# Optimization experiments

Measured on AMD Instinct MI355X. Metric: run time of the kernel, lower is better.

Reference implementation:

```python
import jax, jax.numpy as jnp
import numpy as np

DEPTH = 4
N_MOLS = 2000
ATOMS_PER_MOL = 50
N_ATOMS = N_MOLS * ATOMS_PER_MOL + 1   # +1 zero-padding row (chemprop convention)
N_BONDS = 200001                        # +1 zero-padding row
MAX_NB = 6
ATOM_FDIM, BOND_FDIM, HIDDEN = 133, 147, 300


def setup_inputs() -> dict:
    key = jax.random.key(0)
    ks = jax.random.split(key, 12)
    f_atoms = jax.random.uniform(ks[0], (N_ATOMS, ATOM_FDIM), jnp.float32).at[0].set(0.0)
    f_bonds = jax.random.uniform(ks[1], (N_BONDS, BOND_FDIM), jnp.float32).at[0].set(0.0)
    w_atoms = jax.random.uniform(ks[2], (N_ATOMS,), jnp.float32) + 0.5
    w_bonds = (jax.random.uniform(ks[3], (N_BONDS,), jnp.float32) + 0.5).at[0].set(0.0)
    a2b = jax.random.randint(ks[4], (N_ATOMS, MAX_NB), 0, N_BONDS, jnp.int32)
    b2a = jax.random.randint(ks[5], (N_BONDS,), 0, N_ATOMS, jnp.int32)
    b2revb = jax.random.randint(ks[6], (N_BONDS,), 0, N_BONDS, jnp.int32)
    # segment id per atom; padding atom 0 -> dummy segment N_MOLS (dropped)
    mol_id = jnp.concatenate([jnp.array([N_MOLS], jnp.int32),
                              jnp.repeat(jnp.arange(N_MOLS, dtype=jnp.int32), ATOMS_PER_MOL)])
    degree_of_polym = jax.random.uniform(ks[7], (N_MOLS,), jnp.float32) + 0.5
    s = 0.05
    W_i = jax.random.normal(ks[8], (BOND_FDIM, HIDDEN), jnp.float32) * s
    W_h = jax.random.normal(ks[9], (HIDDEN, HIDDEN), jnp.float32) * s
    W_o = jax.random.normal(ks[10], (ATOM_FDIM + HIDDEN, HIDDEN), jnp.float32) * s
    b_o = jnp.zeros((HIDDEN,), jnp.float32)
    return dict(f_atoms=f_atoms, f_bonds=f_bonds, w_atoms=w_atoms, w_bonds=w_bonds,
                degree_of_polym=degree_of_polym, W_i=W_i, W_h=W_h, W_o=W_o, b_o=b_o,
                a2b=a2b, b2a=b2a, b2revb=b2revb, mol_id=mol_id)


def reference(f_atoms, f_bonds, w_atoms, w_bonds, degree_of_polym,
              W_i, W_h, W_o, b_o, a2b, b2a, b2revb, mol_id):
    # bond-message MPNN (atom_messages=False, undirected=False, ReLU, dropout=0 eval)
    inp = f_bonds @ W_i                                   # [n_bonds, H], no bias
    message = jax.nn.relu(inp)
    for _ in range(DEPTH - 1):
        # gather incoming directed-bond messages per atom and weight them
        nei_msg = message[a2b] * w_bonds[a2b][..., None]  # [n_atoms, max_nb, H]
        a_message = nei_msg.sum(axis=1)                   # [n_atoms, H]
        # subtract reverse message (weighted)
        message = a_message[b2a] - message[b2revb] * w_bonds[:, None]
        message = jax.nn.relu(inp + message @ W_h)
    # final atom aggregation
    nei_msg = message[a2b] * w_bonds[a2b][..., None]
    a_message = nei_msg.sum(axis=1)                       # [n_atoms, H]
    a_input = jnp.concatenate([f_atoms, a_message], axis=1)
    atom_hiddens = jax.nn.relu(a_input @ W_o + b_o)       # [n_atoms, H]
    # per-molecule weighted mean readout, scaled by degree of polymerization
    weighted = w_atoms[:, None] * atom_hiddens
    sums = jax.ops.segment_sum(weighted, mol_id, num_segments=N_MOLS + 1)[:N_MOLS]
    wsum = jax.ops.segment_sum(w_atoms, mol_id, num_segments=N_MOLS + 1)[:N_MOLS]
    mol_vecs = degree_of_polym[:, None] * (sums / wsum[:, None])
    return mol_vecs
```

## Files before the change

kernel.cpp:

```cpp
#include <hip/hip_runtime.h>

#define N_MOLS  2000
#define APM     50
#define N_ATOMS 100001
#define N_BONDS 200001
#define MAX_NB  6
#define AF      133
#define BF      147
#define H       300

#define SB    320
#define SF    160
#define MB_P  200192
#define MA_P  100096
#define SWH   320
#define SWI   160
#define SWO   480

typedef _Float16 f16x8 __attribute__((ext_vector_type(8)));
typedef float    f32x4 __attribute__((ext_vector_type(4)));

__device__ inline unsigned int f16_to_fp8(_Float16 h) {
    union { _Float16 h; unsigned short u; } cv; cv.h = h;
    const unsigned short u = cv.u;
    const int s = (u >> 15) & 1;
    const int e = (u >> 10) & 31;
    const int m = u & 1023;
    int e8 = e - 8;
    if (e8 <= 0) return s << 7;
    int m8 = (m + 64) >> 7;
    if (m8 == 8) { m8 = 0; e8 += 1; }
    if (e8 > 15 || (e8 == 15 && m8 > 6)) return (s << 7) | 0x7E;
    return (s << 7) | (e8 << 3) | m8;
}
__device__ inline float fp8_to_f32(unsigned int c) {
    const int s = (c >> 7) & 1, e = (c >> 3) & 15, m = c & 7;
    if (e == 0) return 0.f;
    union { unsigned short u; _Float16 h; } cv;
    cv.u = (unsigned short)((s << 15) | ((e + 8) << 10) | (m << 7));
    return (float)cv.h;
}

__global__ void cast_fb_kernel(const float* __restrict__ src, _Float16* __restrict__ dst) {
    unsigned i = blockIdx.x * blockDim.x + threadIdx.x;
    if (i >= (unsigned)MB_P * SF) return;
    unsigned m = i / SF, k = i % SF;
    dst[i] = (_Float16)((m < N_BONDS && k < BF) ? src[(size_t)m * BF + k] : 0.f);
}
__global__ void cast_fa_kernel(const float* __restrict__ src, _Float16* __restrict__ dst) {
    unsigned i = blockIdx.x * blockDim.x + threadIdx.x;
    if (i >= (unsigned)MA_P * SF) return;
    unsigned m = i / SF, k = i % SF;
    dst[i] = (_Float16)((m < N_ATOMS && k < AF) ? src[(size_t)m * AF + k] : 0.f);
}
__global__ void cast_wh_kernel(const float* __restrict__ W, _Float16* __restrict__ Wt) {
    int i = blockIdx.x * blockDim.x + threadIdx.x;
    if (i >= 320 * SWH) return;
    int n = i / SWH, k = i % SWH;
    Wt[i] = (_Float16)((n < H && k < H) ? W[k * H + n] : 0.f);
}
__global__ void cast_wi_kernel(const float* __restrict__ W, _Float16* __restrict__ Wt) {
    int i = blockIdx.x * blockDim.x + threadIdx.x;
    if (i >= 320 * SWI) return;
    int n = i / SWI, k = i % SWI;
    Wt[i] = (_Float16)((n < H && k < BF) ? W[k * H + n] : 0.f);
}
__global__ void cast_wo_kernel(const float* __restrict__ W, _Float16* __restrict__ Wt) {
    int i = blockIdx.x * blockDim.x + threadIdx.x;
    if (i >= 320 * SWO) return;
    int n = i / SWO, r = i % SWO;
    float v = 0.f;
    if (n < H) {
        if (r < 320) { if (r < H) v = W[(AF + r) * H + n]; }
        else         { int rr = r - 320; if (rr < AF) v = W[rr * H + n]; }
    }
    Wt[i] = (_Float16)v;
}

template<int NCHUNK, int MODE>
__global__ __launch_bounds__(256, 2) void dgemm_kernel(
    const _Float16* __restrict__ A1, const _Float16* __restrict__ A2,
    const _Float16* __restrict__ Wt, const float* __restrict__ bias,
    _Float16* __restrict__ out16, unsigned char* __restrict__ out8)
{
    constexpr int SW = (MODE == 0) ? SWI : (MODE == 1 ? SWH : SWO);
    __shared__ __align__(16) _Float16 Bs[2][320 * 40];

    const int tid  = threadIdx.x;
    const int lane = tid & 63, wave = tid >> 6;
    const int r16  = lane & 15, quad = lane >> 4;
    const int rowhalf = wave >> 1, colhalf = wave & 1;
    const int row0 = blockIdx.x * 128 + rowhalf * 64;
    const int colb = colhalf * 160;

    #pragma unroll
    for (int i = 0; i < 5; ++i) {
        const int idx = tid + i * 256;
        const int c = idx >> 2, part = idx & 3;
        *(f16x8*)(&Bs[0][c * 40 + part * 8]) =
            *(const f16x8*)(Wt + (size_t)c * SW + part * 8);
    }
    __syncthreads();

    f32x4 acc[4][10];
    #pragma unroll
    for (int s = 0; s < 4; ++s)
        #pragma unroll
        for (int ct = 0; ct < 10; ++ct) acc[s][ct] = f32x4{0.f, 0.f, 0.f, 0.f};

    #pragma unroll
    for (int kc = 0; kc < NCHUNK; ++kc) {
        const int cur = kc & 1;
        f16x8 st[5];
        if (kc + 1 < NCHUNK) {
            #pragma unroll
            for (int i = 0; i < 5; ++i) {
                const int idx = tid + i * 256;
                const int c = idx >> 2, part = idx & 3;
                st[i] = *(const f16x8*)(Wt + (size_t)c * SW + (kc + 1) * 32 + part * 8);
            }
        }
        const _Float16* ap; int kl, sa;
        if (MODE == 2 && kc >= 10) { ap = A2; kl = kc - 10; sa = SF; }
        else                       { ap = A1; kl = kc; sa = (MODE == 0 ? SF : SB); }
        f16x8 a[4];
        #pragma unroll
        for (int s = 0; s < 4; ++s)
            a[s] = *(const f16x8*)(ap + (size_t)(row0 + s * 16 + r16) * sa + kl * 32 + quad * 8);
        #pragma unroll
        for (int ct = 0; ct < 10; ++ct) {
            const f16x8 b = *(const f16x8*)(&Bs[cur][(colb + ct * 16 + r16) * 40 + quad * 8]);
            #pragma unroll
            for (int s = 0; s < 4; ++s)
                acc[s][ct] = __builtin_amdgcn_mfma_f32_16x16x32_f16(a[s], b, acc[s][ct], 0, 0, 0);
        }
        if (kc + 1 < NCHUNK) {
            #pragma unroll
            for (int i = 0; i < 5; ++i) {
                const int idx = tid + i * 256;
                const int c = idx >> 2, part = idx & 3;
                *(f16x8*)(&Bs[cur ^ 1][c * 40 + part * 8]) = st[i];
            }
        }
        __syncthreads();
    }

    #pragma unroll
    for (int ct = 0; ct < 10; ++ct) {
        const int col = colb + ct * 16 + r16;
        const float bv = (MODE == 2 && col < H) ? bias[col] : 0.f;
        #pragma unroll
        for (int s = 0; s < 4; ++s) {
            const int rowb = row0 + s * 16 + quad * 4;
            #pragma unroll
            for (int e = 0; e < 4; ++e) {
                const float v = acc[s][ct][e] + bv;
                const size_t off = (size_t)(rowb + e) * SB + col;
                if (MODE == 0) {
                    out8 [off] = (unsigned char)f16_to_fp8((_Float16)v);
                    out16[off] = (_Float16)(v > 0.f ? v : 0.f);
                } else if (MODE == 1) {
                    out16[off] = (_Float16)v;
                } else {
                    out16[off] = (_Float16)(v > 0.f ? v : 0.f);
                }
            }
        }
    }
}

__global__ __launch_bounds__(256, 8) void aggregate_kernel(
    const _Float16* __restrict__ src,
    const int* __restrict__ a2b,
    const float* __restrict__ w_bonds,
    _Float16* __restrict__ dst)
{
    const int lane = threadIdx.x & 63;
    const int a = blockIdx.x * 4 + (threadIdx.x >> 6);
    if (a >= N_ATOMS || lane >= 40) return;
    const int h0 = lane * 8;
    float acc[8] = {0, 0, 0, 0, 0, 0, 0, 0};
    #pragma unroll
    for (int k = 0; k < MAX_NB; ++k) {
        const int b = a2b[a * MAX_NB + k];
        const float w = w_bonds[b];
        const f16x8 m = *(const f16x8*)(src + (size_t)b * SB + h0);
        #pragma unroll
        for (int j = 0; j < 8; ++j) acc[j] += w * (float)m[j];
    }
    f16x8 o;
    #pragma unroll
    for (int j = 0; j < 8; ++j) o[j] = (_Float16)acc[j];
    *(f16x8*)(dst + (size_t)a * SB + h0) = o;
}

__global__ __launch_bounds__(256, 8) void update_kernel(
    const unsigned char* __restrict__ inp8,
    const _Float16* __restrict__ hm,
    const _Float16* __restrict__ hb,
    const int* __restrict__ b2a,
    const int* __restrict__ b2revb,
    const float* __restrict__ w_bonds,
    _Float16* __restrict__ msg)
{
    const int lane = threadIdx.x & 63;
    const int b = blockIdx.x * 4 + (threadIdx.x >> 6);
    if (b >= MB_P || lane >= 40) return;
    const bool real = b < N_BONDS;
    const int bc = real ? b : 0;
    const int a  = b2a[bc];
    const int rb = b2revb[bc];
    const float w = w_bonds[bc];
    const int h0 = lane * 8;
    const uint2 i8  = *(const uint2*)(inp8 + (size_t)b * SB + h0);
    const f16x8 hmv = *(const f16x8*)(hm + (size_t)a  * SB + h0);
    const f16x8 hbv = *(const f16x8*)(hb + (size_t)rb * SB + h0);
    f16x8 o;
    #pragma unroll
    for (int j = 0; j < 8; ++j) {
        const unsigned int c = ((j < 4 ? i8.x : i8.y) >> (8 * (j & 3))) & 255u;
        const float v = fp8_to_f32(c) + (float)hmv[j] - w * (float)hbv[j];
        o[j] = (_Float16)((real && v > 0.f) ? v : 0.f);
    }
    *(f16x8*)(msg + (size_t)b * SB + h0) = o;
}

__global__ __launch_bounds__(256, 8) void readout_kernel(
    const _Float16* __restrict__ ah,
    const float* __restrict__ w_atoms,
    const float* __restrict__ dop,
    float* __restrict__ out)
{
    const int lane = threadIdx.x & 63;
    const int m = blockIdx.x * 4 + (threadIdx.x >> 6);
    if (m >= N_MOLS || lane >= 40) return;
    const int h0 = lane * 8;
    const int a0 = 1 + m * APM;
    float acc[8] = {0, 0, 0, 0, 0, 0, 0, 0};
    float wsum = 0.f;
    for (int i = 0; i < APM; ++i) {
        const float w = w_atoms[a0 + i];
        wsum += w;
        const f16x8 v = *(const f16x8*)(ah + (size_t)(a0 + i) * SB + h0);
        #pragma unroll
        for (int j = 0; j < 8; ++j) acc[j] += w * (float)v[j];
    }
    const float s = dop[m] / wsum;
    #pragma unroll
    for (int j = 0; j < 8; ++j) {
        const int h = h0 + j;
        if (h < H) out[(size_t)m * H + h] = s * acc[j];
    }
}

extern "C" void kernel_launch(void* const* d_in, const int* in_sizes, int n_in,
                              void* d_out, int out_size, void* d_ws, size_t ws_size,
                              hipStream_t stream) {
    const float* f_atoms = (const float*)d_in[0];
    const float* f_bonds = (const float*)d_in[1];
    const float* w_atoms = (const float*)d_in[2];
    const float* w_bonds = (const float*)d_in[3];
    const float* dop     = (const float*)d_in[4];
    const float* W_i     = (const float*)d_in[5];
    const float* W_h     = (const float*)d_in[6];
    const float* W_o     = (const float*)d_in[7];
    const float* b_o     = (const float*)d_in[8];
    const int* a2b    = (const int*)d_in[9];
    const int* b2a    = (const int*)d_in[10];
    const int* b2revb = (const int*)d_in[11];
    float* out = (float*)d_out;

    char* p = (char*)d_ws;
    auto alloc = [&](size_t bytes) {
        char* q = p;
        p += ((bytes + 64 + 255) / 256) * 256;
        return q;
    };
    unsigned char* inp8 = (unsigned char*)alloc((size_t)MB_P * SB);
    _Float16* msg  = (_Float16*)alloc((size_t)MB_P * SB * 2);
    _Float16* hb   = (_Float16*)alloc((size_t)MB_P * SB * 2);
    _Float16* hm   = (_Float16*)alloc((size_t)MA_P * SB * 2);
    _Float16* Wth  = (_Float16*)alloc((size_t)320 * SWH * 2);
    _Float16* Wti  = (_Float16*)alloc((size_t)320 * SWI * 2);
    _Float16* Wto  = (_Float16*)alloc((size_t)320 * SWO * 2);
    _Float16* fb16 = hb;
    _Float16* fa16 = (_Float16*)inp8;
    _Float16* ah   = hb;

    if ((size_t)(p - (char*)d_ws) > ws_size) {
        hipMemsetAsync(d_out, 0, (size_t)out_size * sizeof(float), stream);
        return;
    }

    {
        unsigned n1 = (unsigned)MB_P * SF;
        cast_fb_kernel<<<(n1 + 255) / 256, 256, 0, stream>>>(f_bonds, fb16);
        cast_wh_kernel<<<(320 * SWH + 255) / 256, 256, 0, stream>>>(W_h, Wth);
        cast_wi_kernel<<<(320 * SWI + 255) / 256, 256, 0, stream>>>(W_i, Wti);
        cast_wo_kernel<<<(320 * SWO + 255) / 256, 256, 0, stream>>>(W_o, Wto);
    }

    const int gB = MB_P / 128;
    const int gA = MA_P / 128;
    const int aggGrid = (N_ATOMS + 3) / 4;
    const int updGrid = MB_P / 4;

    dgemm_kernel<5, 0><<<gB, 256, 0, stream>>>(fb16, nullptr, Wti, nullptr, msg, inp8);
    for (int d = 0; d < 3; ++d) {
        dgemm_kernel<10, 1><<<gB, 256, 0, stream>>>(msg, nullptr, Wth, nullptr, hb, nullptr);
        aggregate_kernel<<<aggGrid, 256, 0, stream>>>(hb, a2b, w_bonds, hm);
        update_kernel<<<updGrid, 256, 0, stream>>>(inp8, hm, hb, b2a, b2revb, w_bonds, msg);
    }
    aggregate_kernel<<<aggGrid, 256, 0, stream>>>(msg, a2b, w_bonds, hm);
    {
        unsigned n2 = (unsigned)MA_P * SF;
        cast_fa_kernel<<<(n2 + 255) / 256, 256, 0, stream>>>(f_atoms, fa16);
    }
    dgemm_kernel<15, 2><<<gA, 256, 0, stream>>>(hm, fa16, Wto, b_o, ah, nullptr);
    readout_kernel<<<(N_MOLS + 3) / 4, 256, 0, stream>>>(ah, w_atoms, dop, out);
}
```

Before: 1.293 ms.

## Stage GEMM epilogue through LDS for vector stores; use hardware FP8 conversions

The GEMM epilogue now writes accumulators into shared memory in four passes and then has each thread emit coalesced 16-byte fp16 and 8-byte fp8 stores, replacing scattered 2-byte and 1-byte global writes. The software fp16-to-fp8 encode and fp8 decode routines are replaced with the cvt_pk_fp8_f32 and cvt_pk_f32_fp8 builtins. The epilogue gains extra block barriers and LDS round trips. The hardware fp8 format may round or saturate differently from the custom E4M3-like encoding.

```diff
diff --git a/kernel.cpp b/kernel.cpp
--- a/kernel.cpp
+++ b/kernel.cpp
@@ -18,28 +18,9 @@
 #define SWO   480
 
 typedef _Float16 f16x8 __attribute__((ext_vector_type(8)));
+typedef _Float16 f16x4 __attribute__((ext_vector_type(4)));
 typedef float    f32x4 __attribute__((ext_vector_type(4)));
-
-__device__ inline unsigned int f16_to_fp8(_Float16 h) {
-    union { _Float16 h; unsigned short u; } cv; cv.h = h;
-    const unsigned short u = cv.u;
-    const int s = (u >> 15) & 1;
-    const int e = (u >> 10) & 31;
-    const int m = u & 1023;
-    int e8 = e - 8;
-    if (e8 <= 0) return s << 7;
-    int m8 = (m + 64) >> 7;
-    if (m8 == 8) { m8 = 0; e8 += 1; }
-    if (e8 > 15 || (e8 == 15 && m8 > 6)) return (s << 7) | 0x7E;
-    return (s << 7) | (e8 << 3) | m8;
-}
-__device__ inline float fp8_to_f32(unsigned int c) {
-    const int s = (c >> 7) & 1, e = (c >> 3) & 15, m = c & 7;
-    if (e == 0) return 0.f;
-    union { unsigned short u; _Float16 h; } cv;
-    cv.u = (unsigned short)((s << 15) | ((e + 8) << 10) | (m << 7));
-    return (float)cv.h;
-}
+typedef float    f32x2 __attribute__((ext_vector_type(2)));
 
 __global__ void cast_fb_kernel(const float* __restrict__ src, _Float16* __restrict__ dst) {
     unsigned i = blockIdx.x * blockDim.x + threadIdx.x;
@@ -145,26 +126,57 @@
         __syncthreads();
     }
 
-    #pragma unroll
-    for (int ct = 0; ct < 10; ++ct) {
-        const int col = colb + ct * 16 + r16;
-        const float bv = (MODE == 2 && col < H) ? bias[col] : 0.f;
-        #pragma unroll
-        for (int s = 0; s < 4; ++s) {
-            const int rowb = row0 + s * 16 + quad * 4;
-            #pragma unroll
-            for (int e = 0; e < 4; ++e) {
-                const float v = acc[s][ct][e] + bv;
-                const size_t off = (size_t)(rowb + e) * SB + col;
-                if (MODE == 0) {
-                    out8 [off] = (unsigned char)f16_to_fp8((_Float16)v);
-                    out16[off] = (_Float16)(v > 0.f ? v : 0.f);
-                } else if (MODE == 1) {
-                    out16[off] = (_Float16)v;
-                } else {
-                    out16[off] = (_Float16)(v > 0.f ? v : 0.f);
+    {
+        _Float16* stage = &Bs[0][0];
+        #pragma unroll
+        for (int p = 0; p < 4; ++p) {
+            if ((p >> 1) == rowhalf) {
+                const int sb0 = (p & 1) * 2;
+                #pragma unroll
+                for (int s2 = 0; s2 < 2; ++s2) {
+                    const int s = sb0 + s2;
+                    #pragma unroll
+                    for (int ct = 0; ct < 10; ++ct) {
+                        const int col = colb + ct * 16 + r16;
+                        const float bv = (MODE == 2 && col < H) ? bias[col] : 0.f;
+                        const int lr = s2 * 16 + quad * 4;
+                        #pragma unroll
+                        for (int e = 0; e < 4; ++e)
+                            stage[(lr + e) * 324 + col] = (_Float16)(acc[s][ct][e] + bv);
+                    }
                 }
             }
+            __syncthreads();
+            #pragma unroll
+            for (int i = 0; i < 5; ++i) {
+                const int c = tid + i * 256;
+                const int row = c / 40, colc = (c % 40) * 8;
+                const _Float16* sp = stage + row * 324 + colc;
+                const f16x4 vlo = *(const f16x4*)(sp);
+                const f16x4 vhi = *(const f16x4*)(sp + 4);
+                f16x8 v;
+                #pragma unroll
+                for (int j = 0; j < 4; ++j) { v[j] = vlo[j]; v[j + 4] = vhi[j]; }
+                const size_t off = (size_t)(blockIdx.x * 128 + p * 32 + row) * SB + colc;
+                if (MODE == 0) {
+                    float f[8];
+                    #pragma unroll
+                    for (int j = 0; j < 8; ++j) f[j] = (float)v[j];
+                    int w0 = __builtin_amdgcn_cvt_pk_fp8_f32(f[0], f[1], 0, false);
+                    w0 = __builtin_amdgcn_cvt_pk_fp8_f32(f[2], f[3], w0, true);
+                    int w1 = __builtin_amdgcn_cvt_pk_fp8_f32(f[4], f[5], 0, false);
+                    w1 = __builtin_amdgcn_cvt_pk_fp8_f32(f[6], f[7], w1, true);
+                    uint2 pk; pk.x = (unsigned int)w0; pk.y = (unsigned int)w1;
+                    *(uint2*)(out8 + off) = pk;
+                }
+                if (MODE == 0 || MODE == 2) {
+                    #pragma unroll
+                    for (int j = 0; j < 8; ++j)
+                        v[j] = (v[j] > (_Float16)0) ? v[j] : (_Float16)0;
+                }
+                *(f16x8*)(out16 + off) = v;
+            }
+            if (p < 3) __syncthreads();
         }
     }
 }
@@ -215,11 +227,15 @@
     const uint2 i8  = *(const uint2*)(inp8 + (size_t)b * SB + h0);
     const f16x8 hmv = *(const f16x8*)(hm + (size_t)a  * SB + h0);
     const f16x8 hbv = *(const f16x8*)(hb + (size_t)rb * SB + h0);
+    const f32x2 d0 = __builtin_amdgcn_cvt_pk_f32_fp8(i8.x, false);
+    const f32x2 d1 = __builtin_amdgcn_cvt_pk_f32_fp8(i8.x, true);
+    const f32x2 d2 = __builtin_amdgcn_cvt_pk_f32_fp8(i8.y, false);
+    const f32x2 d3 = __builtin_amdgcn_cvt_pk_f32_fp8(i8.y, true);
+    const float inpf[8] = {d0[0], d0[1], d1[0], d1[1], d2[0], d2[1], d3[0], d3[1]};
     f16x8 o;
     #pragma unroll
     for (int j = 0; j < 8; ++j) {
-        const unsigned int c = ((j < 4 ? i8.x : i8.y) >> (8 * (j & 3))) & 255u;
-        const float v = fp8_to_f32(c) + (float)hmv[j] - w * (float)hbv[j];
+        const float v = inpf[j] + (float)hmv[j] - w * (float)hbv[j];
         o[j] = (_Float16)((real && v > 0.f) ? v : 0.f);
     }
     *(f16x8*)(msg + (size_t)b * SB + h0) = o;
```

New measurement: 1.172 ms. -9.3%, faster.
